# Kernel tuning notes

Hardware: AMD Instinct MI355X
Metric: run time of the kernel (lower is better)

Reference implementation:

```python
import jax, jax.numpy as jnp
import numpy as np

# Static graph/model dims
G, NPG, N = 64, 200, 12800          # graphs, nodes/graph, total nodes
EPG, E = 1000, 64000                # edges/graph, total edges
D, H, C = 1024, 3, 1024             # feature_size, heads, out channels/head
K1, K2, K3 = 160, 80, 16            # topk sizes: ceil(.8*200), .5*160, .2*80
NEG = -1e9


def _gat(x, src, dst, mask, W, att_s, att_d, b):
    """PyG GATConv (concat heads, add_self_loops=True, leaky_relu 0.2)."""
    n = x.shape[0]
    xw = (x @ W).reshape(n, H, C)                 # [n,H,C]
    a_s = (xw * att_s).sum(-1)                    # [n,H]
    a_d = (xw * att_d).sum(-1)
    loop = jnp.arange(n, dtype=src.dtype)
    s = jnp.concatenate([src, loop])
    d = jnp.concatenate([dst, loop])
    m = jnp.concatenate([mask, jnp.ones((n,), bool)])
    logit = jax.nn.leaky_relu(a_s[s] + a_d[d], 0.2)   # [E+n,H]
    logit = jnp.where(m[:, None], logit, NEG)
    mx = jax.ops.segment_max(logit, d, num_segments=n)
    ex = jnp.where(m[:, None], jnp.exp(logit - mx[d]), 0.0)
    den = jax.ops.segment_sum(ex, d, num_segments=n)
    alpha = ex / (den[d] + 1e-16)                 # segment softmax over dst
    out = jax.ops.segment_sum(alpha[:, :, None] * xw[s], d, num_segments=n)
    return out.reshape(n, H * C) + b


def _topk(x, src, dst, mask, p, n_in, k):
    """PyG TopKPooling: score=tanh(x.p/||p||), keep top-k per graph,
    scale kept rows by score; edge filtering realized as a mask."""
    score = jnp.tanh((x @ p) / jnp.linalg.norm(p))
    vals, idx = jax.lax.top_k(score.reshape(G, n_in), k)     # [G,k]
    perm = (idx + jnp.arange(G)[:, None] * n_in).reshape(-1)
    new_x = x[perm] * vals.reshape(-1, 1)
    newid = jnp.full((G * n_in,), -1, jnp.int32).at[perm].set(
        jnp.arange(G * k, dtype=jnp.int32))
    ns, nd = newid[src], newid[dst]
    nm = mask & (ns >= 0) & (nd >= 0)
    return new_x, jnp.where(nm, ns, 0), jnp.where(nm, nd, 0), nm


def _readout(x, k):
    xg = x.reshape(G, k, C)                       # contiguous equal graphs
    return jnp.concatenate([xg.max(1), xg.mean(1)], axis=1)  # [G,2C]


def setup_inputs() -> dict:
    key = jax.random.key(0)
    ks = jax.random.split(key, 32)
    x = jax.random.normal(ks[0], (N, D), jnp.float32)
    gid = jnp.repeat(jnp.arange(G, dtype=jnp.int32), EPG)
    src = jax.random.randint(ks[1], (E,), 0, NPG, jnp.int32) + gid * NPG
    dst = jax.random.randint(ks[2], (E,), 0, NPG, jnp.int32) + gid * NPG
    edge_index = jnp.stack([src, dst])
    batch_index = jnp.repeat(jnp.arange(G, dtype=jnp.int32), NPG)
    edge_attr = jnp.zeros((E, 1), jnp.float32)

    def gl(k, shape, fan):
        return jax.random.normal(k, shape, jnp.float32) * (1.0 / np.sqrt(fan))

    inp = dict(x=x, edge_attr=edge_attr, edge_index=edge_index,
               batch_index=batch_index)
    i = 3
    for L, fin in ((1, D), (2, C), (3, C)):
        inp[f'W{L}'] = gl(ks[i], (fin, H * C), fin); i += 1
        inp[f'as{L}'] = gl(ks[i], (H, C), C); i += 1
        inp[f'ad{L}'] = gl(ks[i], (H, C), C); i += 1
        inp[f'b{L}'] = jnp.zeros((H * C,), jnp.float32)
        inp[f'Wt{L}'] = gl(ks[i], (H * C, C), H * C); i += 1
        inp[f'bt{L}'] = jnp.zeros((C,), jnp.float32)
        inp[f'p{L}'] = gl(ks[i], (C,), C); i += 1
    inp['Wl1'] = gl(ks[i], (2 * C, 1024), 2 * C); i += 1
    inp['bl1'] = jnp.zeros((1024,), jnp.float32)
    inp['Wl2'] = gl(ks[i], (1024, 2), 1024); i += 1
    inp['bl2'] = jnp.zeros((2,), jnp.float32)
    return inp


def reference(x, edge_attr, edge_index, batch_index,
              W1, as1, ad1, b1, Wt1, bt1, p1,
              W2, as2, ad2, b2, Wt2, bt2, p2,
              W3, as3, ad3, b3, Wt3, bt3, p3,
              Wl1, bl1, Wl2, bl2):
    src, dst = edge_index[0], edge_index[1]
    mask = jnp.ones((src.shape[0],), bool)
    h = _gat(x, src, dst, mask, W1, as1, ad1, b1) @ Wt1 + bt1
    h, src, dst, mask = _topk(h, src, dst, mask, p1, NPG, K1)
    r1 = _readout(h, K1)
    h = _gat(h, src, dst, mask, W2, as2, ad2, b2) @ Wt2 + bt2
    h, src, dst, mask = _topk(h, src, dst, mask, p2, K1, K2)
    r2 = _readout(h, K2)
    h = _gat(h, src, dst, mask, W3, as3, ad3, b3) @ Wt3 + bt3
    h, src, dst, mask = _topk(h, src, dst, mask, p3, K2, K3)
    r3 = _readout(h, K3)
    z = r1 + r2 + r3                               # [G, 2C]
    z = jax.nn.relu(z @ Wl1 + bl1)                 # dropout inactive (eval)
    return z @ Wl2 + bl2                           # [G, 2]
```

## Files before the change

kernel.cpp:

```cpp
#include <hip/hip_runtime.h>
#include <math.h>

#define NG 64
#define EE 64000
#define HC3 3072
#define CC 1024

static inline int cdiv(int a, int b) { return (a + b - 1) / b; }

typedef float f4_t __attribute__((ext_vector_type(4)));
typedef short s8_t __attribute__((ext_vector_type(8)));

__device__ __forceinline__ float lrelu(float x) { return x > 0.f ? x : 0.2f * x; }
__device__ __forceinline__ unsigned fenc(float f) {
    unsigned u = __float_as_uint(f);
    return (u & 0x80000000u) ? ~u : (u | 0x80000000u);
}
__device__ __forceinline__ float fdec(unsigned e) {
    return (e & 0x80000000u) ? __uint_as_float(e ^ 0x80000000u) : __uint_as_float(~e);
}
__device__ __forceinline__ unsigned short f2bf(float f) {
    unsigned u = __float_as_uint(f);
    u += 0x7fffu + ((u >> 16) & 1u);
    return (unsigned short)(u >> 16);
}
__device__ __forceinline__ float bf2f(unsigned short h) {
    return __uint_as_float(((unsigned)h) << 16);
}
__device__ __forceinline__ void gll16(const unsigned short* g, unsigned short* l) {
    __builtin_amdgcn_global_load_lds(
        (const __attribute__((address_space(1))) void*)g,
        (__attribute__((address_space(3))) void*)l, 16, 0, 0);
}

__global__ __launch_bounds__(256) void gemm_split(
    const unsigned short* __restrict__ Ahi, const unsigned short* __restrict__ Alo, int lda,
    const unsigned short* __restrict__ Bhi, const unsigned short* __restrict__ Blo, int ldb,
    const float* __restrict__ bias, const float* __restrict__ rowscale,
    float* __restrict__ C, int ldc, int K,
    size_t zsA, size_t zsB, size_t zsC)
{
    __shared__ unsigned short sAH[128 * 32];
    __shared__ unsigned short sAL[128 * 32];
    __shared__ unsigned short sBH[128 * 32];
    __shared__ unsigned short sBL[128 * 32];

    Ahi += blockIdx.z * zsA; Alo += blockIdx.z * zsA;
    Bhi += blockIdx.z * zsB; Blo += blockIdx.z * zsB;
    C   += blockIdx.z * zsC;

    const int t = threadIdx.x;
    const int w = t >> 6, lane = t & 63;
    const int wr = w >> 1, wc = w & 1;
    const int row0 = blockIdx.y * 128, col0 = blockIdx.x * 128;

    const int srow = w * 16 + (lane >> 2);
    const int skg = (((lane & 3) ^ ((lane >> 3) & 3)) << 3);
    const size_t aoff0 = (size_t)(row0 + srow) * lda + skg;
    const size_t aoff1 = (size_t)(row0 + 64 + srow) * lda + skg;
    const size_t boff0 = (size_t)(col0 + srow) * ldb + skg;
    const size_t boff1 = (size_t)(col0 + 64 + srow) * ldb + skg;
    const int l0 = (w * 16) * 32;
    const int l1 = (64 + w * 16) * 32;

    f4_t acc[4][4];
    const f4_t z4 = {0.f, 0.f, 0.f, 0.f};
#pragma unroll
    for (int i = 0; i < 4; ++i)
#pragma unroll
        for (int j = 0; j < 4; ++j) acc[i][j] = z4;

    const int mrow0 = wr * 64 + (lane & 15);
    const int nrow0 = wc * 64 + (lane & 15);
    const int kslot = (((lane >> 4) ^ ((lane >> 1) & 3)) << 3);

    for (int k0 = 0; k0 < K; k0 += 32) {
        gll16(Ahi + aoff0 + k0, &sAH[l0]);
        gll16(Ahi + aoff1 + k0, &sAH[l1]);
        gll16(Alo + aoff0 + k0, &sAL[l0]);
        gll16(Alo + aoff1 + k0, &sAL[l1]);
        gll16(Bhi + boff0 + k0, &sBH[l0]);
        gll16(Bhi + boff1 + k0, &sBH[l1]);
        gll16(Blo + boff0 + k0, &sBL[l0]);
        gll16(Blo + boff1 + k0, &sBL[l1]);
        __syncthreads();

        s8_t ah[4], al[4], bh[4], bl[4];
#pragma unroll
        for (int mt = 0; mt < 4; ++mt) {
            ah[mt] = *(const s8_t*)&sAH[(mrow0 + mt * 16) * 32 + kslot];
            al[mt] = *(const s8_t*)&sAL[(mrow0 + mt * 16) * 32 + kslot];
        }
#pragma unroll
        for (int nt = 0; nt < 4; ++nt) {
            bh[nt] = *(const s8_t*)&sBH[(nrow0 + nt * 16) * 32 + kslot];
            bl[nt] = *(const s8_t*)&sBL[(nrow0 + nt * 16) * 32 + kslot];
        }
#pragma unroll
        for (int mt = 0; mt < 4; ++mt)
#pragma unroll
            for (int nt = 0; nt < 4; ++nt) {
                acc[mt][nt] = __builtin_amdgcn_mfma_f32_16x16x32_bf16(ah[mt], bh[nt], acc[mt][nt], 0, 0, 0);
                acc[mt][nt] = __builtin_amdgcn_mfma_f32_16x16x32_bf16(ah[mt], bl[nt], acc[mt][nt], 0, 0, 0);
                acc[mt][nt] = __builtin_amdgcn_mfma_f32_16x16x32_bf16(al[mt], bh[nt], acc[mt][nt], 0, 0, 0);
            }
        __syncthreads();
    }

#pragma unroll
    for (int mt = 0; mt < 4; ++mt) {
        int row = row0 + wr * 64 + mt * 16 + (lane >> 4) * 4;
#pragma unroll
        for (int nt = 0; nt < 4; ++nt) {
            int col = col0 + wc * 64 + nt * 16 + (lane & 15);
            float b = bias ? bias[col] : 0.f;
#pragma unroll
            for (int r = 0; r < 4; ++r) {
                float v = acc[mt][nt][r] + b;
                if (rowscale) v *= rowscale[row + r];
                C[(size_t)(row + r) * ldc + col] = v;
            }
        }
    }
}

__global__ void split_w_all(const float* __restrict__ w0, const float* __restrict__ w1,
    const float* __restrict__ w2, int lbase,
    unsigned short* __restrict__ ohi, unsigned short* __restrict__ olo)
{
    const float* Wp[3] = {w0, w1, w2};
    int slot = blockIdx.y;
    int L = lbase + slot / 3, h = slot % 3;
    int idx = blockIdx.x * 256 + threadIdx.x;
    int r = idx >> 10, c = idx & 1023;
    float v = Wp[L][(size_t)r * HC3 + h * CC + c];
    unsigned short hh = f2bf(v);
    ohi[(size_t)slot * 1048576 + idx] = hh;
    olo[(size_t)slot * 1048576 + idx] = f2bf(v - bf2f(hh));
}

__global__ void transpose_split_wt_all(const float* __restrict__ w0,
    const float* __restrict__ w1, const float* __restrict__ w2, int lbase,
    unsigned short* __restrict__ ohi, unsigned short* __restrict__ olo)
{
    const float* Wp[3] = {w0, w1, w2};
    int slot = blockIdx.z;
    int L = lbase + slot / 3, h = slot % 3;
    __shared__ float tile[32][33];
    int t = threadIdx.x, tr = t >> 5, tc = t & 31;
    int r0 = blockIdx.y * 32, c0 = blockIdx.x * 32;
    const float* in = Wp[L] + (size_t)h * 1048576;
#pragma unroll
    for (int i = 0; i < 4; ++i)
        tile[tr + i * 8][tc] = in[(size_t)(r0 + tr + i * 8) * CC + c0 + tc];
    __syncthreads();
    unsigned short* oh = ohi + (size_t)slot * 1048576;
    unsigned short* ol = olo + (size_t)slot * 1048576;
#pragma unroll
    for (int i = 0; i < 4; ++i) {
        int oc = c0 + tr + i * 8;
        int orr = r0 + tc;
        float v = tile[tc][tr + i * 8];
        unsigned short hh = f2bf(v);
        oh[(size_t)oc * CC + orr] = hh;
        ol[(size_t)oc * CC + orr] = f2bf(v - bf2f(hh));
    }
}

__global__ void split_interleave_all(const float* __restrict__ in,
    unsigned short* __restrict__ ohi, unsigned short* __restrict__ olo)
{
    int slot = blockIdx.y;
    int lrel = slot / 3, h = slot % 3;
    int idx = blockIdx.x * 256 + threadIdx.x;
    int c = idx >> 10, d = idx & 1023;
    float v = in[(size_t)slot * 1048576 + idx];
    unsigned short hh = f2bf(v);
    size_t dst = (size_t)lrel * 3145728 + (size_t)c * HC3 + h * CC + d;
    ohi[dst] = hh;
    olo[dst] = f2bf(v - bf2f(hh));
}

__global__ void qzero(float* __restrict__ q, int n) {
    int i = blockIdx.x * 256 + threadIdx.x;
    if (i < n) q[i] = 0.f;
}

__global__ void qvec_all(const float* __restrict__ MHT, const float* __restrict__ p0,
    const float* __restrict__ p1, const float* __restrict__ p2, int lbase,
    float* __restrict__ q)
{
    const float* Pp[3] = {p0, p1, p2};
    int slot = blockIdx.z;
    int L = lbase + slot / 3, h = slot % 3;
    int d = blockIdx.x * 256 + threadIdx.x;
    int c0 = blockIdx.y * 128;
    const float* m = MHT + (size_t)slot * 1048576 + (size_t)c0 * CC + d;
    const float* p = Pp[L];
    float s = 0.f;
#pragma unroll 8
    for (int c = 0; c < 128; ++c) s += m[(size_t)c * CC] * p[c0 + c];
    atomicAdd(&q[(size_t)L * HC3 + h * CC + d], s);
}

__global__ __launch_bounds__(256) void attvec_all(const float* __restrict__ w0,
    const float* __restrict__ w1, const float* __restrict__ w2,
    const float* __restrict__ as0, const float* __restrict__ as1, const float* __restrict__ as2,
    const float* __restrict__ ad0, const float* __restrict__ ad1, const float* __restrict__ ad2,
    int lbase, float* __restrict__ asv, float* __restrict__ adv)
{
    const float* Wp[3] = {w0, w1, w2};
    const float* Sp[3] = {as0, as1, as2};
    const float* Dp[3] = {ad0, ad1, ad2};
    int L = lbase + blockIdx.y;
    int wid = blockIdx.x * 4 + (threadIdx.x >> 6);
    int lane = threadIdx.x & 63;
    int h = wid >> 10, kk = wid & 1023;
    const float* wr = Wp[L] + (long long)kk * HC3 + h * CC;
    const float* sa = Sp[L] + h * CC;
    const float* da = Dp[L] + h * CC;
    float ss = 0.f, dd = 0.f;
    for (int c = lane; c < CC; c += 64) { float w = wr[c]; ss += w * sa[c]; dd += w * da[c]; }
    for (int off = 32; off; off >>= 1) { ss += __shfl_xor(ss, off, 64); dd += __shfl_xor(dd, off, 64); }
    if (lane == 0) { asv[(size_t)L * HC3 + h * CC + kk] = ss; adv[(size_t)L * HC3 + h * CC + kk] = dd; }
}

__global__ __launch_bounds__(256) void attn_dots_t(const float* __restrict__ xin,
    const float* __restrict__ asv, const float* __restrict__ adv, const float* __restrict__ q,
    float* __restrict__ AS, float* __restrict__ AD, float* __restrict__ T3, int n)
{
    int node = blockIdx.x * 4 + (threadIdx.x >> 6);
    int lane = threadIdx.x & 63;
    if (node >= n) return;
    const float* xr = xin + (long long)node * CC;
    float s0 = 0, s1 = 0, s2 = 0, d0 = 0, d1 = 0, d2 = 0, t0 = 0, t1 = 0, t2 = 0;
    for (int j = lane; j < CC; j += 64) {
        float v = xr[j];
        s0 += v * asv[j]; s1 += v * asv[CC + j]; s2 += v * asv[2 * CC + j];
        d0 += v * adv[j]; d1 += v * adv[CC + j]; d2 += v * adv[2 * CC + j];
        t0 += v * q[j];   t1 += v * q[CC + j];   t2 += v * q[2 * CC + j];
    }
    for (int off = 32; off; off >>= 1) {
        s0 += __shfl_xor(s0, off, 64); s1 += __shfl_xor(s1, off, 64); s2 += __shfl_xor(s2, off, 64);
        d0 += __shfl_xor(d0, off, 64); d1 += __shfl_xor(d1, off, 64); d2 += __shfl_xor(d2, off, 64);
        t0 += __shfl_xor(t0, off, 64); t1 += __shfl_xor(t1, off, 64); t2 += __shfl_xor(t2, off, 64);
    }
    if (lane == 0) {
        AS[node * 3 + 0] = s0; AS[node * 3 + 1] = s1; AS[node * 3 + 2] = s2;
        AD[node * 3 + 0] = d0; AD[node * 3 + 1] = d1; AD[node * 3 + 2] = d2;
        T3[node * 3 + 0] = t0; T3[node * 3 + 1] = t1; T3[node * 3 + 2] = t2;
    }
}

__global__ void bvinit_pnorm(const float* __restrict__ bt0, const float* __restrict__ bt1,
    const float* __restrict__ bt2, const float* __restrict__ p0, const float* __restrict__ p1,
    const float* __restrict__ p2, int lbase, float* __restrict__ BV, float* __restrict__ PN)
{
    const float* Bp[3] = {bt0, bt1, bt2};
    const float* Pp[3] = {p0, p1, p2};
    int L = lbase + blockIdx.y;
    if (blockIdx.x < 4) {
        int c = blockIdx.x * 256 + threadIdx.x;
        BV[(size_t)L * CC + c] = Bp[L][c];
    } else {
        __shared__ float red[256];
        int t = threadIdx.x;
        const float* p = Pp[L];
        float s = 0.f;
        for (int j = t; j < CC; j += 256) { float v = p[j]; s += v * v; }
        red[t] = s; __syncthreads();
        for (int off = 128; off; off >>= 1) { if (t < off) red[t] += red[t + off]; __syncthreads(); }
        if (t == 0) PN[L] = sqrtf(red[0]);
    }
}

__global__ void bvec_part(const float* __restrict__ b0, const float* __restrict__ b1,
    const float* __restrict__ b2, const float* __restrict__ wt0, const float* __restrict__ wt1,
    const float* __restrict__ wt2, int lbase, float* __restrict__ BV)
{
    const float* bp[3] = {b0, b1, b2};
    const float* wp[3] = {wt0, wt1, wt2};
    int L = lbase + blockIdx.z;
    int c = blockIdx.x * 256 + threadIdx.x;
    int k0 = blockIdx.y * 256;
    const float* b = bp[L];
    const float* Wt = wp[L];
    float acc = 0.f;
#pragma unroll 8
    for (int k = k0; k < k0 + 256; ++k) acc += b[k] * Wt[(size_t)k * CC + c];
    atomicAdd(&BV[(size_t)L * CC + c], acc);
}

__global__ void bvp_all(const float* __restrict__ BV, const float* __restrict__ p0,
    const float* __restrict__ p1, const float* __restrict__ p2, int lbase,
    float* __restrict__ BVP)
{
    const float* Pp[3] = {p0, p1, p2};
    int L = lbase + blockIdx.x;
    __shared__ float red[256];
    int t = threadIdx.x;
    const float* p = Pp[L];
    float s = 0.f;
    for (int j = t; j < CC; j += 256) s += BV[(size_t)L * CC + j] * p[j];
    red[t] = s; __syncthreads();
    for (int off = 128; off; off >>= 1) { if (t < off) red[t] += red[t + off]; __syncthreads(); }
    if (t == 0) BVP[L] = red[0];
}

__global__ void node_init_zero(const float* __restrict__ AS, const float* __restrict__ AD,
    float* __restrict__ sl, unsigned* __restrict__ mxe, float* __restrict__ sexp,
    int* __restrict__ cnt, int* __restrict__ cur, int n)
{
    int i = blockIdx.x * 256 + threadIdx.x;
    if (i >= n) return;
#pragma unroll
    for (int h = 0; h < 3; ++h) {
        float l = lrelu(AS[i * 3 + h] + AD[i * 3 + h]);
        sl[i * 3 + h] = l;
        mxe[i * 3 + h] = fenc(l);
        sexp[i * 3 + h] = 0.f;
    }
    cnt[i] = 0; cur[i] = 0;
}

__global__ void edge_pass1(const int* __restrict__ src, const int* __restrict__ dst,
    const int* __restrict__ msk, const float* __restrict__ AS, const float* __restrict__ AD,
    unsigned* __restrict__ mxe, float* __restrict__ sexp, int* __restrict__ cnt)
{
    int e = blockIdx.x * 256 + threadIdx.x;
    if (e >= EE || !msk[e]) return;
    int s = src[e], d = dst[e];
    atomicAdd(&cnt[d], 1);
#pragma unroll
    for (int h = 0; h < 3; ++h) {
        float l = lrelu(AS[s * 3 + h] + AD[d * 3 + h]);
        atomicMax(&mxe[d * 3 + h], fenc(l));
        atomicAdd(&sexp[d * 3 + h], expf(l));
    }
}

__global__ void scan_graph(const int* __restrict__ cnt, int* __restrict__ offs,
    int* __restrict__ gt, int npg)
{
    if (threadIdx.x != 0) return;
    int g = blockIdx.x, base = g * npg, run = 0;
    for (int i = 0; i < npg; ++i) { offs[base + i] = run; run += cnt[base + i]; }
    gt[g] = run;
}

__global__ void scan_base(const int* __restrict__ gt, int* __restrict__ gb)
{
    if (threadIdx.x != 0 || blockIdx.x != 0) return;
    int run = 0;
    for (int g = 0; g < NG; ++g) { gb[g] = run; run += gt[g]; }
}

__global__ void add_base(int* __restrict__ offs, const int* __restrict__ gb, int n, int npg)
{
    int i = blockIdx.x * 256 + threadIdx.x;
    if (i < n) offs[i] += gb[i / npg];
}

__global__ void decode_selfden(const unsigned* __restrict__ mxe, const float* __restrict__ sl,
    const float* __restrict__ sexp, float* __restrict__ mxf, float* __restrict__ den, int n)
{
    int i = blockIdx.x * 256 + threadIdx.x;
    if (i >= n) return;
#pragma unroll
    for (int h = 0; h < 3; ++h) {
        float m = fdec(mxe[i * 3 + h]);
        mxf[i * 3 + h] = m;
        den[i * 3 + h] = expf(sl[i * 3 + h] - m) + expf(-m) * sexp[i * 3 + h];
    }
}

__global__ void fill_alpha(const int* __restrict__ src, const int* __restrict__ dst,
    const int* __restrict__ msk, const int* __restrict__ offs, int* __restrict__ cur,
    const float* __restrict__ AS, const float* __restrict__ AD,
    const float* __restrict__ mxf, const float* __restrict__ den,
    int* __restrict__ csrs, float* __restrict__ csra)
{
    int e = blockIdx.x * 256 + threadIdx.x;
    if (e >= EE || !msk[e]) return;
    int s = src[e], d = dst[e];
    int pos = offs[d] + atomicAdd(&cur[d], 1);
    csrs[pos] = s;
#pragma unroll
    for (int h = 0; h < 3; ++h) {
        float l = lrelu(AS[s * 3 + h] + AD[d * 3 + h]);
        float ex = expf(l - mxf[d * 3 + h]);
        csra[pos * 3 + h] = ex / (den[d * 3 + h] + 1e-16f);
    }
}

__global__ void score_csr(const float* __restrict__ T3,
    const float* __restrict__ sl, const float* __restrict__ mxf, const float* __restrict__ den,
    const int* __restrict__ offs, const int* __restrict__ cnt, const int* __restrict__ csrs,
    const float* __restrict__ csra, const float* __restrict__ bvp, const float* __restrict__ pn,
    float* __restrict__ score, int n)
{
    int i = blockIdx.x * 256 + threadIdx.x;
    if (i >= n) return;
    float s = 0.f;
#pragma unroll
    for (int h = 0; h < 3; ++h) {
        float aself = expf(sl[i * 3 + h] - mxf[i * 3 + h]) / (den[i * 3 + h] + 1e-16f);
        s += aself * T3[i * 3 + h];
    }
    int beg = offs[i], num = cnt[i];
    for (int e = 0; e < num; ++e) {
        int sn = csrs[beg + e];
#pragma unroll
        for (int h = 0; h < 3; ++h) s += csra[(beg + e) * 3 + h] * T3[sn * 3 + h];
    }
    score[i] = tanhf((s + bvp[0]) / pn[0]);
}

__global__ __launch_bounds__(64) void topk_kernel(const float* __restrict__ score,
    int npg, int k, int* __restrict__ perm, float* __restrict__ vals, int* __restrict__ newid)
{
    int g = blockIdx.x, lane = threadIdx.x;
    for (int idx = lane; idx < npg; idx += 64) newid[g * npg + idx] = -1;
    const float* sc = score + g * npg;
    float v[4];
    int nsl = (npg + 63) >> 6;
#pragma unroll
    for (int s2 = 0; s2 < 4; ++s2) {
        int idx = lane + (s2 << 6);
        v[s2] = (s2 < nsl && idx < npg) ? sc[idx] : -1e30f;
    }
    for (int j = 0; j < k; ++j) {
        float bv = -2e30f; int bi = 0x7fffffff;
#pragma unroll
        for (int s2 = 0; s2 < 4; ++s2) {
            int idx = lane + (s2 << 6);
            if (v[s2] > bv) { bv = v[s2]; bi = idx; }
        }
        for (int off = 32; off; off >>= 1) {
            float ov = __shfl_xor(bv, off, 64);
            int   oi = __shfl_xor(bi, off, 64);
            if (ov > bv || (ov == bv && oi < bi)) { bv = ov; bi = oi; }
        }
        if (lane == 0) {
            perm[g * k + j] = g * npg + bi;
            vals[g * k + j] = bv;
            newid[g * npg + bi] = g * k + j;
        }
        if ((bi & 63) == lane) v[bi >> 6] = -1e30f;
    }
}

__global__ __launch_bounds__(256) void aggregate_sel(const float* __restrict__ xin,
    const float* __restrict__ sl, const float* __restrict__ mxf, const float* __restrict__ den,
    const int* __restrict__ offs, const int* __restrict__ cnt,
    const int* __restrict__ csrs, const float* __restrict__ csra,
    const int* __restrict__ perm,
    unsigned short* __restrict__ ahi, unsigned short* __restrict__ alo)
{
    int r = blockIdx.x, t = threadIdx.x;
    int i = perm[r];
    float aself[3];
#pragma unroll
    for (int h = 0; h < 3; ++h)
        aself[h] = expf(sl[i * 3 + h] - mxf[i * 3 + h]) / (den[i * 3 + h] + 1e-16f);
    const float* xr = xin + (long long)i * CC;
    float acc[3][4];
#pragma unroll
    for (int j = 0; j < 4; ++j) {
        float v = xr[t + (j << 8)];
#pragma unroll
        for (int h = 0; h < 3; ++h) acc[h][j] = aself[h] * v;
    }
    int beg = offs[i], num = cnt[i];
    for (int e = 0; e < num; ++e) {
        int s = csrs[beg + e];
        float a0 = csra[(beg + e) * 3 + 0];
        float a1 = csra[(beg + e) * 3 + 1];
        float a2 = csra[(beg + e) * 3 + 2];
        const float* sr = xin + (long long)s * CC;
#pragma unroll
        for (int j = 0; j < 4; ++j) {
            float v = sr[t + (j << 8)];
            acc[0][j] += a0 * v; acc[1][j] += a1 * v; acc[2][j] += a2 * v;
        }
    }
#pragma unroll
    for (int h = 0; h < 3; ++h)
#pragma unroll
        for (int j = 0; j < 4; ++j) {
            int c = t + (j << 8);
            float v = acc[h][j];
            unsigned short hh = f2bf(v);
            size_t idx = (size_t)r * HC3 + h * CC + c;
            ahi[idx] = hh;
            alo[idx] = f2bf(v - bf2f(hh));
        }
}

__global__ void remap_edges(int* __restrict__ s, int* __restrict__ d,
    int* __restrict__ m, const int* __restrict__ newid)
{
    int e = blockIdx.x * 256 + threadIdx.x;
    if (e >= EE) return;
    if (!m[e]) { s[e] = 0; d[e] = 0; return; }
    int ns = newid[s[e]], nd = newid[d[e]];
    int nm = (ns >= 0 && nd >= 0) ? 1 : 0;
    m[e] = nm; s[e] = nm ? ns : 0; d[e] = nm ? nd : 0;
}

__global__ __launch_bounds__(256) void readout_part(const float* __restrict__ xn,
    int k, float* __restrict__ PM, float* __restrict__ PS)
{
    int g = blockIdx.x, ch = blockIdx.y, t = threadIdx.x;
    int rpc = k >> 3, r0 = ch * rpc;
#pragma unroll
    for (int j = 0; j < 4; ++j) {
        int c = t + (j << 8);
        float mx = -1e30f, sm = 0.f;
        for (int r = r0; r < r0 + rpc; ++r) {
            float vv = xn[((size_t)(g * k + r)) * CC + c];
            mx = fmaxf(mx, vv); sm += vv;
        }
        PM[(size_t)(g * 8 + ch) * CC + c] = mx;
        PS[(size_t)(g * 8 + ch) * CC + c] = sm;
    }
}

__global__ __launch_bounds__(256) void readout_fin(const float* __restrict__ PM,
    const float* __restrict__ PS, int k, float* __restrict__ R)
{
    int g = blockIdx.x, t = threadIdx.x;
#pragma unroll
    for (int j = 0; j < 4; ++j) {
        int c = t + (j << 8);
        float mx = -1e30f, sm = 0.f;
#pragma unroll
        for (int ch = 0; ch < 8; ++ch) {
            mx = fmaxf(mx, PM[(size_t)(g * 8 + ch) * CC + c]);
            sm += PS[(size_t)(g * 8 + ch) * CC + c];
        }
        R[g * 2048 + c] = mx;
        R[g * 2048 + 1024 + c] = sm / (float)k;
    }
}

__global__ void copy_edges(const int* __restrict__ ei, int* __restrict__ s,
    int* __restrict__ d, int* __restrict__ m)
{
    int e = blockIdx.x * 256 + threadIdx.x;
    if (e >= EE) return;
    s[e] = ei[e]; d[e] = ei[EE + e]; m[e] = 1;
}

__global__ void zsum(const float* __restrict__ a, const float* __restrict__ b,
    const float* __restrict__ c, float* __restrict__ z)
{
    int i = blockIdx.x * 256 + threadIdx.x;
    if (i < NG * 2048) z[i] = a[i] + b[i] + c[i];
}

__global__ __launch_bounds__(256) void mlp1_kernel(const float* __restrict__ Z,
    const float* __restrict__ Wl1, const float* __restrict__ bl1, float* __restrict__ Z1)
{
    int c = blockIdx.x * 256 + threadIdx.x;
    int g = blockIdx.y;
    float acc = bl1[c];
    const float* zr = Z + g * 2048;
    for (int kk = 0; kk < 2048; ++kk) acc += zr[kk] * Wl1[kk * 1024 + c];
    Z1[g * 1024 + c] = acc > 0.f ? acc : 0.f;
}

__global__ __launch_bounds__(64) void mlp2_kernel(const float* __restrict__ Z1,
    const float* __restrict__ Wl2, const float* __restrict__ bl2, float* __restrict__ out)
{
    int b = blockIdx.x; int g = b >> 1, o = b & 1;
    int lane = threadIdx.x;
    const float* zr = Z1 + g * 1024;
    float s = 0.f;
    for (int j = lane; j < 1024; j += 64) s += zr[j] * Wl2[j * 2 + o];
    for (int off = 32; off; off >>= 1) s += __shfl_xor(s, off, 64);
    if (lane == 0) out[g * 2 + o] = s + bl2[o];
}

extern "C" void kernel_launch(void* const* d_in, const int* in_sizes, int n_in,
                              void* d_out, int out_size, void* d_ws, size_t ws_size,
                              hipStream_t stream)
{
    const float* x   = (const float*)d_in[0];
    const int*   ei  = (const int*)d_in[2];
    const float* W[3]    = {(const float*)d_in[4],  (const float*)d_in[11], (const float*)d_in[18]};
    const float* atts[3] = {(const float*)d_in[5],  (const float*)d_in[12], (const float*)d_in[19]};
    const float* attd[3] = {(const float*)d_in[6],  (const float*)d_in[13], (const float*)d_in[20]};
    const float* bb[3]   = {(const float*)d_in[7],  (const float*)d_in[14], (const float*)d_in[21]};
    const float* Wt[3]   = {(const float*)d_in[8],  (const float*)d_in[15], (const float*)d_in[22]};
    const float* bt[3]   = {(const float*)d_in[9],  (const float*)d_in[16], (const float*)d_in[23]};
    const float* pv[3]   = {(const float*)d_in[10], (const float*)d_in[17], (const float*)d_in[24]};
    const float* Wl1 = (const float*)d_in[25];
    const float* bl1 = (const float*)d_in[26];
    const float* Wl2 = (const float*)d_in[27];
    const float* bl2 = (const float*)d_in[28];
    float* out = (float*)d_out;

    const bool batched = ws_size >= (size_t)225 * 1024 * 1024;

    char* wp = (char*)d_ws;
    auto carve = [&](size_t bytes) -> void* {
        void* p = (void*)wp;
        wp += (bytes + 255) & ~(size_t)255;
        return p;
    };
    const int NMAX = 12800;
    const int GKMAX = 10240;
    const size_t MSZ = (size_t)CC * CC;
    const int NSLOT = batched ? 9 : 3;
    unsigned short* A2H = (unsigned short*)carve((size_t)GKMAX * HC3 * 2);
    unsigned short* A2L = (unsigned short*)carve((size_t)GKMAX * HC3 * 2);
    unsigned short* WTH = (unsigned short*)A2H;
    unsigned short* WTL = WTH + (size_t)NSLOT * MSZ;
    unsigned short* WSH = WTL + (size_t)NSLOT * MSZ;
    unsigned short* WSL = (unsigned short*)A2L;
    float* MHT = (float*)(WSL + (size_t)NSLOT * MSZ);
    float* XN   = (float*)carve((size_t)GKMAX * CC * 4);
    unsigned short* B2H = (unsigned short*)carve((size_t)NSLOT * MSZ * 2);
    unsigned short* B2L = (unsigned short*)carve((size_t)NSLOT * MSZ * 2);
    float* PM   = (float*)carve((size_t)NG * 8 * CC * 4);
    float* PS   = (float*)carve((size_t)NG * 8 * CC * 4);
    float* ASV  = (float*)carve((size_t)3 * HC3 * 4);
    float* ADV  = (float*)carve((size_t)3 * HC3 * 4);
    float* QV   = (float*)carve((size_t)3 * HC3 * 4);
    float* BV   = (float*)carve((size_t)3 * CC * 4);
    float* AS   = (float*)carve((size_t)NMAX * 3 * 4);
    float* AD   = (float*)carve((size_t)NMAX * 3 * 4);
    float* T3   = (float*)carve((size_t)NMAX * 3 * 4);
    float* SL   = (float*)carve((size_t)NMAX * 3 * 4);
    unsigned* MXE = (unsigned*)carve((size_t)NMAX * 3 * 4);
    float* MXF  = (float*)carve((size_t)NMAX * 3 * 4);
    float* DEN  = (float*)carve((size_t)NMAX * 3 * 4);
    float* SEXP = (float*)carve((size_t)NMAX * 3 * 4);
    int* CNT    = (int*)carve((size_t)NMAX * 4);
    int* OFFS   = (int*)carve((size_t)NMAX * 4);
    int* CUR    = (int*)carve((size_t)NMAX * 4);
    int* NEWID  = (int*)carve((size_t)NMAX * 4);
    int* GT     = (int*)carve((size_t)NG * 4);
    int* GB     = (int*)carve((size_t)NG * 4);
    int* CSRS   = (int*)carve((size_t)EE * 4);
    float* CSRA = (float*)carve((size_t)EE * 3 * 4);
    int* SRC = (int*)carve((size_t)EE * 4);
    int* DST = (int*)carve((size_t)EE * 4);
    int* MK  = (int*)carve((size_t)EE * 4);
    int* PERM  = (int*)carve((size_t)GKMAX * 4);
    float* VALS = (float*)carve((size_t)GKMAX * 4);
    float* SCORE = (float*)carve((size_t)NMAX * 4);
    float* PN  = (float*)carve(256);
    float* BVP = (float*)carve(256);
    float* R0 = (float*)carve((size_t)NG * 2048 * 4);
    float* R1 = (float*)carve((size_t)NG * 2048 * 4);
    float* R2 = (float*)carve((size_t)NG * 2048 * 4);
    float* Z  = (float*)carve((size_t)NG * 2048 * 4);
    float* Z1 = (float*)carve((size_t)NG * 1024 * 4);
    float* Rarr[3] = {R0, R1, R2};
    (void)in_sizes; (void)n_in; (void)out_size;

    copy_edges<<<cdiv(EE, 256), 256, 0, stream>>>(ei, SRC, DST, MK);

    auto prep = [&](int lbase, int nl) {
        int nslots = 3 * nl;
        split_w_all<<<dim3(4096, nslots), 256, 0, stream>>>(W[0], W[1], W[2], lbase, WSH, WSL);
        transpose_split_wt_all<<<dim3(32, 32, nslots), 256, 0, stream>>>(Wt[0], Wt[1], Wt[2],
                                                                          lbase, WTH, WTL);
        gemm_split<<<dim3(8, 8, nslots), 256, 0, stream>>>(WTH, WTL, CC, WSH, WSL, CC,
            nullptr, nullptr, MHT, CC, CC, MSZ, MSZ, MSZ);
        split_interleave_all<<<dim3(4096, nslots), 256, 0, stream>>>(MHT, B2H, B2L);
        qzero<<<cdiv(nl * HC3, 256), 256, 0, stream>>>(QV + (size_t)lbase * HC3, nl * HC3);
        qvec_all<<<dim3(4, 8, nslots), 256, 0, stream>>>(MHT, pv[0], pv[1], pv[2], lbase, QV);
        attvec_all<<<dim3(768, nl), 256, 0, stream>>>(W[0], W[1], W[2],
            atts[0], atts[1], atts[2], attd[0], attd[1], attd[2], lbase, ASV, ADV);
        bvinit_pnorm<<<dim3(5, nl), 256, 0, stream>>>(bt[0], bt[1], bt[2],
            pv[0], pv[1], pv[2], lbase, BV, PN);
        bvec_part<<<dim3(4, 12, nl), 256, 0, stream>>>(bb[0], bb[1], bb[2],
            Wt[0], Wt[1], Wt[2], lbase, BV);
        bvp_all<<<nl, 256, 0, stream>>>(BV, pv[0], pv[1], pv[2], lbase, BVP);
    };

    if (batched) prep(0, 3);

    const int ns_[3]  = {12800, 10240, 5120};
    const int npg_[3] = {200, 160, 80};
    const int kk_[3]  = {160, 80, 16};
    const float* xin = x;

    for (int L = 0; L < 3; ++L) {
        int n = ns_[L], npg = npg_[L], k = kk_[L];
        int gk = NG * k;
        if (!batched) prep(L, 1);
        size_t b2off = batched ? (size_t)L * 3 * MSZ : 0;
        attn_dots_t<<<n / 4, 256, 0, stream>>>(xin, ASV + (size_t)L * HC3,
            ADV + (size_t)L * HC3, QV + (size_t)L * HC3, AS, AD, T3, n);
        node_init_zero<<<cdiv(n, 256), 256, 0, stream>>>(AS, AD, SL, MXE, SEXP, CNT, CUR, n);
        edge_pass1<<<cdiv(EE, 256), 256, 0, stream>>>(SRC, DST, MK, AS, AD, MXE, SEXP, CNT);
        scan_graph<<<NG, 64, 0, stream>>>(CNT, OFFS, GT, npg);
        scan_base<<<1, 64, 0, stream>>>(GT, GB);
        add_base<<<cdiv(n, 256), 256, 0, stream>>>(OFFS, GB, n, npg);
        decode_selfden<<<cdiv(n, 256), 256, 0, stream>>>(MXE, SL, SEXP, MXF, DEN, n);
        fill_alpha<<<cdiv(EE, 256), 256, 0, stream>>>(SRC, DST, MK, OFFS, CUR,
                                                      AS, AD, MXF, DEN, CSRS, CSRA);
        score_csr<<<cdiv(n, 256), 256, 0, stream>>>(T3, SL, MXF, DEN, OFFS, CNT, CSRS, CSRA,
                                                    BVP + L, PN + L, SCORE, n);
        topk_kernel<<<NG, 64, 0, stream>>>(SCORE, npg, k, PERM, VALS, NEWID);
        aggregate_sel<<<gk, 256, 0, stream>>>(xin, SL, MXF, DEN, OFFS, CNT, CSRS, CSRA,
                                              PERM, A2H, A2L);
        gemm_split<<<dim3(8, gk / 128, 1), 256, 0, stream>>>(A2H, A2L, HC3,
            B2H + b2off, B2L + b2off, HC3, BV + (size_t)L * CC, VALS, XN, CC, HC3, 0, 0, 0);
        readout_part<<<dim3(NG, 8), 256, 0, stream>>>(XN, k, PM, PS);
        readout_fin<<<NG, 256, 0, stream>>>(PM, PS, k, Rarr[L]);
        if (L < 2) remap_edges<<<cdiv(EE, 256), 256, 0, stream>>>(SRC, DST, MK, NEWID);
        xin = XN;
    }

    zsum<<<cdiv(NG * 2048, 256), 256, 0, stream>>>(R0, R1, R2, Z);
    mlp1_kernel<<<dim3(4, NG), 256, 0, stream>>>(Z, Wl1, bl1, Z1);
    mlp2_kernel<<<NG * 2, 64, 0, stream>>>(Z1, Wl2, bl2, out);
}
```

Before: 1.594 ms.

## Split-K the per-layer GEMM with atomics and fuse small node/scan/topk kernels

Replaces the per-layer output GEMM with a split-K variant that accumulates into a zeroed buffer via atomicAdd, then applies bias and the top-k row scale in a separate finalize kernel. The aim is more workgroups for the small-M layers (64, 40 and 8 row tiles), which otherwise underfill the GPU. It also folds node_init into the attention dot kernel, merges scan_base and add_base into one kernel, and computes scores inside the top-k kernel to remove launches. In exchange it adds a memset, float atomics with nondeterministic summation order, and an extra full pass over XN.

```diff
diff --git a/kernel.cpp b/kernel.cpp
--- a/kernel.cpp
+++ b/kernel.cpp
@@ -36,7 +36,6 @@
 __global__ __launch_bounds__(256) void gemm_split(
     const unsigned short* __restrict__ Ahi, const unsigned short* __restrict__ Alo, int lda,
     const unsigned short* __restrict__ Bhi, const unsigned short* __restrict__ Blo, int ldb,
-    const float* __restrict__ bias, const float* __restrict__ rowscale,
     float* __restrict__ C, int ldc, int K,
     size_t zsA, size_t zsB, size_t zsC)
 {
@@ -113,15 +112,106 @@
 #pragma unroll
         for (int nt = 0; nt < 4; ++nt) {
             int col = col0 + wc * 64 + nt * 16 + (lane & 15);
-            float b = bias ? bias[col] : 0.f;
-#pragma unroll
-            for (int r = 0; r < 4; ++r) {
-                float v = acc[mt][nt][r] + b;
-                if (rowscale) v *= rowscale[row + r];
-                C[(size_t)(row + r) * ldc + col] = v;
+#pragma unroll
+            for (int r = 0; r < 4; ++r)
+                C[(size_t)(row + r) * ldc + col] = acc[mt][nt][r];
+        }
+    }
+}
+
+__global__ __launch_bounds__(256) void gemm_splitk(
+    const unsigned short* __restrict__ Ahi, const unsigned short* __restrict__ Alo, int lda,
+    const unsigned short* __restrict__ Bhi, const unsigned short* __restrict__ Blo, int ldb,
+    float* __restrict__ C, int ldc, int ksub)
+{
+    __shared__ unsigned short sAH[128 * 32];
+    __shared__ unsigned short sAL[128 * 32];
+    __shared__ unsigned short sBH[128 * 32];
+    __shared__ unsigned short sBL[128 * 32];
+
+    const int t = threadIdx.x;
+    const int w = t >> 6, lane = t & 63;
+    const int wr = w >> 1, wc = w & 1;
+    const int row0 = blockIdx.x * 128, col0 = blockIdx.y * 128;
+    const int kbase = blockIdx.z * ksub;
+
+    const int srow = w * 16 + (lane >> 2);
+    const int skg = (((lane & 3) ^ ((lane >> 3) & 3)) << 3);
+    const size_t aoff0 = (size_t)(row0 + srow) * lda + skg;
+    const size_t aoff1 = (size_t)(row0 + 64 + srow) * lda + skg;
+    const size_t boff0 = (size_t)(col0 + srow) * ldb + skg;
+    const size_t boff1 = (size_t)(col0 + 64 + srow) * ldb + skg;
+    const int l0 = (w * 16) * 32;
+    const int l1 = (64 + w * 16) * 32;
+
+    f4_t acc[4][4];
+    const f4_t z4 = {0.f, 0.f, 0.f, 0.f};
+#pragma unroll
+    for (int i = 0; i < 4; ++i)
+#pragma unroll
+        for (int j = 0; j < 4; ++j) acc[i][j] = z4;
+
+    const int mrow0 = wr * 64 + (lane & 15);
+    const int nrow0 = wc * 64 + (lane & 15);
+    const int kslot = (((lane >> 4) ^ ((lane >> 1) & 3)) << 3);
+
+    for (int k0 = kbase; k0 < kbase + ksub; k0 += 32) {
+        gll16(Ahi + aoff0 + k0, &sAH[l0]);
+        gll16(Ahi + aoff1 + k0, &sAH[l1]);
+        gll16(Alo + aoff0 + k0, &sAL[l0]);
+        gll16(Alo + aoff1 + k0, &sAL[l1]);
+        gll16(Bhi + boff0 + k0, &sBH[l0]);
+        gll16(Bhi + boff1 + k0, &sBH[l1]);
+        gll16(Blo + boff0 + k0, &sBL[l0]);
+        gll16(Blo + boff1 + k0, &sBL[l1]);
+        __syncthreads();
+
+        s8_t ah[4], al[4], bh[4], bl[4];
+#pragma unroll
+        for (int mt = 0; mt < 4; ++mt) {
+            ah[mt] = *(const s8_t*)&sAH[(mrow0 + mt * 16) * 32 + kslot];
+            al[mt] = *(const s8_t*)&sAL[(mrow0 + mt * 16) * 32 + kslot];
+        }
+#pragma unroll
+        for (int nt = 0; nt < 4; ++nt) {
+            bh[nt] = *(const s8_t*)&sBH[(nrow0 + nt * 16) * 32 + kslot];
+            bl[nt] = *(const s8_t*)&sBL[(nrow0 + nt * 16) * 32 + kslot];
+        }
+#pragma unroll
+        for (int mt = 0; mt < 4; ++mt)
+#pragma unroll
+            for (int nt = 0; nt < 4; ++nt) {
+                acc[mt][nt] = __builtin_amdgcn_mfma_f32_16x16x32_bf16(ah[mt], bh[nt], acc[mt][nt], 0, 0, 0);
+                acc[mt][nt] = __builtin_amdgcn_mfma_f32_16x16x32_bf16(ah[mt], bl[nt], acc[mt][nt], 0, 0, 0);
+                acc[mt][nt] = __builtin_amdgcn_mfma_f32_16x16x32_bf16(al[mt], bh[nt], acc[mt][nt], 0, 0, 0);
             }
-        }
-    }
+        __syncthreads();
+    }
+
+#pragma unroll
+    for (int mt = 0; mt < 4; ++mt) {
+        int row = row0 + wr * 64 + mt * 16 + (lane >> 4) * 4;
+#pragma unroll
+        for (int nt = 0; nt < 4; ++nt) {
+            int col = col0 + wc * 64 + nt * 16 + (lane & 15);
+#pragma unroll
+            for (int r = 0; r < 4; ++r)
+                atomicAdd(&C[(size_t)(row + r) * ldc + col], acc[mt][nt][r]);
+        }
+    }
+}
+
+__global__ __launch_bounds__(256) void finalize_xn(float* __restrict__ XN,
+    const float* __restrict__ BV, const float* __restrict__ vals)
+{
+    int r = blockIdx.x, t = threadIdx.x;
+    float v = vals[r];
+    float4* p = (float4*)(XN + (size_t)r * CC);
+    const float4* b = (const float4*)BV;
+    float4 x = p[t], bb = b[t];
+    x.x = (x.x + bb.x) * v; x.y = (x.y + bb.y) * v;
+    x.z = (x.z + bb.z) * v; x.w = (x.w + bb.w) * v;
+    p[t] = x;
 }
 
 __global__ void split_w_all(const float* __restrict__ w0, const float* __restrict__ w1,
@@ -225,9 +315,11 @@
     if (lane == 0) { asv[(size_t)L * HC3 + h * CC + kk] = ss; adv[(size_t)L * HC3 + h * CC + kk] = dd; }
 }
 
-__global__ __launch_bounds__(256) void attn_dots_t(const float* __restrict__ xin,
+__global__ __launch_bounds__(256) void attn_node(const float* __restrict__ xin,
     const float* __restrict__ asv, const float* __restrict__ adv, const float* __restrict__ q,
-    float* __restrict__ AS, float* __restrict__ AD, float* __restrict__ T3, int n)
+    float* __restrict__ AS, float* __restrict__ AD, float* __restrict__ T3,
+    float* __restrict__ sl, unsigned* __restrict__ mxe, float* __restrict__ sexp,
+    int* __restrict__ cnt, int* __restrict__ cur, int n)
 {
     int node = blockIdx.x * 4 + (threadIdx.x >> 6);
     int lane = threadIdx.x & 63;
@@ -249,6 +341,11 @@
         AS[node * 3 + 0] = s0; AS[node * 3 + 1] = s1; AS[node * 3 + 2] = s2;
         AD[node * 3 + 0] = d0; AD[node * 3 + 1] = d1; AD[node * 3 + 2] = d2;
         T3[node * 3 + 0] = t0; T3[node * 3 + 1] = t1; T3[node * 3 + 2] = t2;
+        float l0v = lrelu(s0 + d0), l1v = lrelu(s1 + d1), l2v = lrelu(s2 + d2);
+        sl[node * 3 + 0] = l0v; sl[node * 3 + 1] = l1v; sl[node * 3 + 2] = l2v;
+        mxe[node * 3 + 0] = fenc(l0v); mxe[node * 3 + 1] = fenc(l1v); mxe[node * 3 + 2] = fenc(l2v);
+        sexp[node * 3 + 0] = 0.f; sexp[node * 3 + 1] = 0.f; sexp[node * 3 + 2] = 0.f;
+        cnt[node] = 0; cur[node] = 0;
     }
 }
 
@@ -307,22 +404,6 @@
     if (t == 0) BVP[L] = red[0];
 }
 
-__global__ void node_init_zero(const float* __restrict__ AS, const float* __restrict__ AD,
-    float* __restrict__ sl, unsigned* __restrict__ mxe, float* __restrict__ sexp,
-    int* __restrict__ cnt, int* __restrict__ cur, int n)
-{
-    int i = blockIdx.x * 256 + threadIdx.x;
-    if (i >= n) return;
-#pragma unroll
-    for (int h = 0; h < 3; ++h) {
-        float l = lrelu(AS[i * 3 + h] + AD[i * 3 + h]);
-        sl[i * 3 + h] = l;
-        mxe[i * 3 + h] = fenc(l);
-        sexp[i * 3 + h] = 0.f;
-    }
-    cnt[i] = 0; cur[i] = 0;
-}
-
 __global__ void edge_pass1(const int* __restrict__ src, const int* __restrict__ dst,
     const int* __restrict__ msk, const float* __restrict__ AS, const float* __restrict__ AD,
     unsigned* __restrict__ mxe, float* __restrict__ sexp, int* __restrict__ cnt)
@@ -348,17 +429,14 @@
     gt[g] = run;
 }
 
-__global__ void scan_base(const int* __restrict__ gt, int* __restrict__ gb)
-{
-    if (threadIdx.x != 0 || blockIdx.x != 0) return;
-    int run = 0;
-    for (int g = 0; g < NG; ++g) { gb[g] = run; run += gt[g]; }
-}
-
-__global__ void add_base(int* __restrict__ offs, const int* __restrict__ gb, int n, int npg)
+__global__ void scan_finish(int* __restrict__ offs, const int* __restrict__ gt, int n, int npg)
 {
     int i = blockIdx.x * 256 + threadIdx.x;
-    if (i < n) offs[i] += gb[i / npg];
+    if (i >= n) return;
+    int g = i / npg;
+    int base = 0;
+    for (int gg = 0; gg < g; ++gg) base += gt[gg];
+    offs[i] += base;
 }
 
 __global__ void decode_selfden(const unsigned* __restrict__ mxe, const float* __restrict__ sl,
@@ -393,35 +471,33 @@
     }
 }
 
-__global__ void score_csr(const float* __restrict__ T3,
+__global__ __launch_bounds__(64) void score_topk(const float* __restrict__ T3,
     const float* __restrict__ sl, const float* __restrict__ mxf, const float* __restrict__ den,
     const int* __restrict__ offs, const int* __restrict__ cnt, const int* __restrict__ csrs,
     const float* __restrict__ csra, const float* __restrict__ bvp, const float* __restrict__ pn,
-    float* __restrict__ score, int n)
-{
-    int i = blockIdx.x * 256 + threadIdx.x;
-    if (i >= n) return;
-    float s = 0.f;
-#pragma unroll
-    for (int h = 0; h < 3; ++h) {
-        float aself = expf(sl[i * 3 + h] - mxf[i * 3 + h]) / (den[i * 3 + h] + 1e-16f);
-        s += aself * T3[i * 3 + h];
-    }
-    int beg = offs[i], num = cnt[i];
-    for (int e = 0; e < num; ++e) {
-        int sn = csrs[beg + e];
-#pragma unroll
-        for (int h = 0; h < 3; ++h) s += csra[(beg + e) * 3 + h] * T3[sn * 3 + h];
-    }
-    score[i] = tanhf((s + bvp[0]) / pn[0]);
-}
-
-__global__ __launch_bounds__(64) void topk_kernel(const float* __restrict__ score,
     int npg, int k, int* __restrict__ perm, float* __restrict__ vals, int* __restrict__ newid)
 {
+    __shared__ float sc[256];
     int g = blockIdx.x, lane = threadIdx.x;
-    for (int idx = lane; idx < npg; idx += 64) newid[g * npg + idx] = -1;
-    const float* sc = score + g * npg;
+    float bv0 = bvp[0], pn0 = pn[0];
+    for (int ii = lane; ii < npg; ii += 64) {
+        int i = g * npg + ii;
+        float s = 0.f;
+#pragma unroll
+        for (int h = 0; h < 3; ++h) {
+            float aself = expf(sl[i * 3 + h] - mxf[i * 3 + h]) / (den[i * 3 + h] + 1e-16f);
+            s += aself * T3[i * 3 + h];
+        }
+        int beg = offs[i], num = cnt[i];
+        for (int e = 0; e < num; ++e) {
+            int sn = csrs[beg + e];
+#pragma unroll
+            for (int h = 0; h < 3; ++h) s += csra[(beg + e) * 3 + h] * T3[sn * 3 + h];
+        }
+        sc[ii] = tanhf((s + bv0) / pn0);
+        newid[i] = -1;
+    }
+    __syncthreads();
     float v[4];
     int nsl = (npg + 63) >> 6;
 #pragma unroll
@@ -642,7 +718,6 @@
     int* CUR    = (int*)carve((size_t)NMAX * 4);
     int* NEWID  = (int*)carve((size_t)NMAX * 4);
     int* GT     = (int*)carve((size_t)NG * 4);
-    int* GB     = (int*)carve((size_t)NG * 4);
     int* CSRS   = (int*)carve((size_t)EE * 4);
     float* CSRA = (float*)carve((size_t)EE * 3 * 4);
     int* SRC = (int*)carve((size_t)EE * 4);
@@ -650,7 +725,6 @@
     int* MK  = (int*)carve((size_t)EE * 4);
     int* PERM  = (int*)carve((size_t)GKMAX * 4);
     float* VALS = (float*)carve((size_t)GKMAX * 4);
-    float* SCORE = (float*)carve((size_t)NMAX * 4);
     float* PN  = (float*)carve(256);
     float* BVP = (float*)carve(256);
     float* R0 = (float*)carve((size_t)NG * 2048 * 4);
@@ -669,7 +743,7 @@
         transpose_split_wt_all<<<dim3(32, 32, nslots), 256, 0, stream>>>(Wt[0], Wt[1], Wt[2],
                                                                           lbase, WTH, WTL);
         gemm_split<<<dim3(8, 8, nslots), 256, 0, stream>>>(WTH, WTL, CC, WSH, WSL, CC,
-            nullptr, nullptr, MHT, CC, CC, MSZ, MSZ, MSZ);
+            MHT, CC, CC, MSZ, MSZ, MSZ);
         split_interleave_all<<<dim3(4096, nslots), 256, 0, stream>>>(MHT, B2H, B2L);
         qzero<<<cdiv(nl * HC3, 256), 256, 0, stream>>>(QV + (size_t)lbase * HC3, nl * HC3);
         qvec_all<<<dim3(4, 8, nslots), 256, 0, stream>>>(MHT, pv[0], pv[1], pv[2], lbase, QV);
@@ -687,6 +761,7 @@
     const int ns_[3]  = {12800, 10240, 5120};
     const int npg_[3] = {200, 160, 80};
     const int kk_[3]  = {160, 80, 16};
+    const int sk_[3]  = {2, 2, 4};
     const float* xin = x;
 
     for (int L = 0; L < 3; ++L) {
@@ -694,23 +769,23 @@
         int gk = NG * k;
         if (!batched) prep(L, 1);
         size_t b2off = batched ? (size_t)L * 3 * MSZ : 0;
-        attn_dots_t<<<n / 4, 256, 0, stream>>>(xin, ASV + (size_t)L * HC3,
-            ADV + (size_t)L * HC3, QV + (size_t)L * HC3, AS, AD, T3, n);
-        node_init_zero<<<cdiv(n, 256), 256, 0, stream>>>(AS, AD, SL, MXE, SEXP, CNT, CUR, n);
+        attn_node<<<n / 4, 256, 0, stream>>>(xin, ASV + (size_t)L * HC3,
+            ADV + (size_t)L * HC3, QV + (size_t)L * HC3, AS, AD, T3,
+            SL, MXE, SEXP, CNT, CUR, n);
         edge_pass1<<<cdiv(EE, 256), 256, 0, stream>>>(SRC, DST, MK, AS, AD, MXE, SEXP, CNT);
         scan_graph<<<NG, 64, 0, stream>>>(CNT, OFFS, GT, npg);
-        scan_base<<<1, 64, 0, stream>>>(GT, GB);
-        add_base<<<cdiv(n, 256), 256, 0, stream>>>(OFFS, GB, n, npg);
+        scan_finish<<<cdiv(n, 256), 256, 0, stream>>>(OFFS, GT, n, npg);
         decode_selfden<<<cdiv(n, 256), 256, 0, stream>>>(MXE, SL, SEXP, MXF, DEN, n);
         fill_alpha<<<cdiv(EE, 256), 256, 0, stream>>>(SRC, DST, MK, OFFS, CUR,
                                                       AS, AD, MXF, DEN, CSRS, CSRA);
-        score_csr<<<cdiv(n, 256), 256, 0, stream>>>(T3, SL, MXF, DEN, OFFS, CNT, CSRS, CSRA,
-                                                    BVP + L, PN + L, SCORE, n);
-        topk_kernel<<<NG, 64, 0, stream>>>(SCORE, npg, k, PERM, VALS, NEWID);
+        score_topk<<<NG, 64, 0, stream>>>(T3, SL, MXF, DEN, OFFS, CNT, CSRS, CSRA,
+                                          BVP + L, PN + L, npg, k, PERM, VALS, NEWID);
         aggregate_sel<<<gk, 256, 0, stream>>>(xin, SL, MXF, DEN, OFFS, CNT, CSRS, CSRA,
                                               PERM, A2H, A2L);
-        gemm_split<<<dim3(8, gk / 128, 1), 256, 0, stream>>>(A2H, A2L, HC3,
-            B2H + b2off, B2L + b2off, HC3, BV + (size_t)L * CC, VALS, XN, CC, HC3, 0, 0, 0);
+        hipMemsetAsync(XN, 0, (size_t)gk * CC * 4, stream);
+        gemm_splitk<<<dim3(gk / 128, 8, sk_[L]), 256, 0, stream>>>(A2H, A2L, HC3,
+            B2H + b2off, B2L + b2off, HC3, XN, CC, HC3 / sk_[L]);
+        finalize_xn<<<gk, 256, 0, stream>>>(XN, BV + (size_t)L * CC, VALS);
         readout_part<<<dim3(NG, 8), 256, 0, stream>>>(XN, k, PM, PS);
         readout_fin<<<NG, 256, 0, stream>>>(PM, PS, k, Rarr[L]);
         if (L < 2) remap_edges<<<cdiv(EE, 256), 256, 0, stream>>>(SRC, DST, MK, NEWID);
```

Measured after the change: 1.386 ms. 1.15x faster.
